# Kernel optimization log

Hardware: AMD Instinct MI355X
Metric: run time of the kernel (lower is better)

The kernel has to match this reference:

```python
import math
import jax, jax.numpy as jnp
import numpy as np

B, S, D, E, K, H = 4, 1024, 768, 8, 2, 2048
NH_ROUTER, NH_COLLAB = 12, 2  # collab heads = min(n_heads, top_k) = 2
EPS = 1e-5


def setup_inputs() -> dict:
    key = jax.random.key(0)
    ks = jax.random.split(key, 16)
    n = lambda k, shp, s=0.02: jax.random.normal(k, shp, jnp.float32) * s
    return {
        "x": jax.random.normal(ks[0], (B, S, D), jnp.float32),
        # parallel expert params (E, D, H) / (E, H, D)
        "w1": n(ks[1], (E, D, H)), "w3": n(ks[2], (E, D, H)), "w2": n(ks[3], (E, H, D)),
        # router self-attention (torch MultiheadAttention packed qkv + out proj)
        "r_in_w": n(ks[4], (3 * D, D)), "r_in_b": jnp.zeros((3 * D,), jnp.float32),
        "r_out_w": n(ks[5], (D, D)), "r_out_b": jnp.zeros((D,), jnp.float32),
        "r_norm_w": jnp.ones((D,), jnp.float32),
        "gate_w": n(ks[6], (E, D)),
        # collaborative cross-attention
        "c_in_w": n(ks[7], (3 * D, D)), "c_in_b": jnp.zeros((3 * D,), jnp.float32),
        "c_out_w": n(ks[8], (D, D)), "c_out_b": jnp.zeros((D,), jnp.float32),
        "c_norm_w": jnp.ones((D,), jnp.float32),
        "ffn_w1": n(ks[9], (D, D)), "ffn_w2": n(ks[10], (D, D)),
        "o_w": n(ks[11], (D, D)),
    }


def _mha(x, in_w, in_b, out_w, out_b, nh):
    # torch nn.MultiheadAttention, batch_first, q=k=v=x; returns out and head-avg probs
    N, L, Dm = x.shape
    hd = Dm // nh
    qkv = x @ in_w.T + in_b                       # (N, L, 3D)
    q, k, v = jnp.split(qkv, 3, axis=-1)
    sp = lambda t: t.reshape(N, L, nh, hd).transpose(0, 2, 1, 3)
    q, k, v = sp(q), sp(k), sp(v)
    probs = jax.nn.softmax(jnp.einsum('nhld,nhmd->nhlm', q, k) / math.sqrt(hd), axis=-1)
    o = jnp.einsum('nhlm,nhmd->nhld', probs, v).transpose(0, 2, 1, 3).reshape(N, L, Dm)
    return o @ out_w.T + out_b, probs.mean(axis=1)


def _rms(x, w):
    return x * jax.lax.rsqrt(jnp.mean(x * x, axis=-1, keepdims=True) + EPS) * w


def reference(x, w1, w3, w2, r_in_w, r_in_b, r_out_w, r_out_b, r_norm_w, gate_w,
              c_in_w, c_in_b, c_out_w, c_out_b, c_norm_w, ffn_w1, ffn_w2, o_w):
    Bx, Sx, Dx = x.shape
    # dense all-expert SwiGLU: (B,S,E,D)
    gate = jnp.einsum('bsd,edh->bseh', x, w1)
    up = jnp.einsum('bsd,edh->bseh', x, w3)
    expert_out = jnp.einsum('bseh,ehd->bsed', jax.nn.silu(gate) * up, w2)
    ef = expert_out.reshape(Bx * Sx, E, Dx)
    # attention-based router over the E experts per token
    ctx, _ = _mha(ef, r_in_w, r_in_b, r_out_w, r_out_b, NH_ROUTER)
    ctx = _rms(ctx + ef, r_norm_w)
    logits = (ctx.mean(axis=1) @ gate_w.T).reshape(Bx, Sx, E)
    routing_probs = jax.nn.softmax(logits, axis=-1)
    tk_logits, tk_idx = jax.lax.top_k(logits, K)  # router_temperature = 1.0
    tk_probs = jax.nn.softmax(tk_logits, axis=-1)
    sel = jnp.take_along_axis(expert_out, tk_idx[..., None], axis=2)  # (B,S,K,D)
    sf = sel.reshape(Bx * Sx, K, Dx)
    # collaborative fusion among selected experts
    ao, aw = _mha(sf, c_in_w, c_in_b, c_out_w, c_out_b, NH_COLLAB)
    ao = _rms(ao + sf, c_norm_w)
    refined = (jax.nn.gelu(ao @ ffn_w1.T, approximate=False) @ ffn_w2.T) + ao
    refined = refined.reshape(Bx, Sx, K, Dx)
    final = jnp.sum(refined * tk_probs[..., None], axis=2) @ o_w.T
    # auxiliary loss
    usage = routing_probs.mean(axis=(0, 1))
    balance = jnp.mean((usage - usage.mean()) ** 2)
    diversity = jnp.mean(-jnp.sum(aw * jnp.log(aw + 1e-9), axis=-1))
    aux = 0.1 * (0.01 * diversity + 0.01 * balance)
    return final, aux, tk_idx
```

## Files before the change

### kernel.cpp

```cpp
#include <hip/hip_runtime.h>


typedef unsigned short u16;
typedef unsigned int u32;
typedef _Float16 f16;
typedef f16 f16x4 __attribute__((ext_vector_type(4)));
typedef f16 f16x8 __attribute__((ext_vector_type(8)));
typedef float f32x4 __attribute__((ext_vector_type(4)));

__device__ __forceinline__ float b2f(u16 v){
  union { u32 u; float f; } x; x.u = ((u32)v) << 16; return x.f;
}
__device__ __forceinline__ u16 f2b(float f){
  union { float f; u32 u; } x; x.f = f;
  u32 u = x.u;
  if ((u & 0x7fffffffu) > 0x7f800000u) return (u16)0x7fc0;
  return (u16)((u + 0x7fffu + ((u >> 16) & 1u)) >> 16);
}
__device__ __forceinline__ float gelu_f(float x){
  return 0.5f * x * (1.f + erff(x * 0.70710678118654752f));
}

template<int NW>
__device__ __forceinline__ float blockReduceSum(float v, float* red){
  #pragma unroll
  for (int o = 32; o > 0; o >>= 1) v += __shfl_down(v, o, 64);
  const int wv = threadIdx.x >> 6, ln = threadIdx.x & 63;
  __syncthreads();
  if (ln == 0) red[wv] = v;
  __syncthreads();
  float s = 0.f;
  #pragma unroll
  for (int i = 0; i < NW; i++) s += red[i];
  return s;
}

template<int AK, bool SPLIT, bool BT, bool BIAS, int ACT, bool RES, bool DUAL, bool SK2>
__global__ __launch_bounds__(256, 2) void mgemm(
    const void* __restrict__ Ap, int lda, long long strideA,
    const float* __restrict__ B1, const float* __restrict__ B2, int ldb, long long strideB,
    float* __restrict__ C1, float* __restrict__ C2, int ldc, long long strideC,
    const float* __restrict__ bias, const float* __restrict__ resid, int ldr,
    int Kd, int zs)
{
  __shared__ f16 AsH[2][128*40];
  __shared__ f16 BsH[2][128*40];
  __shared__ f16 AsL[SPLIT ? 2 : 1][SPLIT ? 128*40 : 4];
  __shared__ f16 BsL[SPLIT ? 2 : 1][SPLIT ? 128*40 : 4];

  const int tid = threadIdx.x;
  const int m0 = blockIdx.y * 128, n0 = blockIdx.x * 128;
  const int z = blockIdx.z;
  int zi = z, k0 = 0, KL = Kd;
  const float* Bz; float* Cz;
  if constexpr (DUAL){
    if (z < zs){ zi = z;      Bz = B1 + (long long)zi*strideB; Cz = C1 + (long long)zi*strideC; }
    else       { zi = z - zs; Bz = B2 + (long long)zi*strideB; Cz = C2 + (long long)zi*strideC; }
  } else if constexpr (SK2){
    const int s = (z >= zs) ? 1 : 0;
    zi = z - s * zs;
    KL = Kd >> 1; k0 = s * KL;
    Bz = B1 + (long long)zi*strideB + (BT ? (long long)k0 : (long long)k0 * ldb);
    Cz = (s ? C2 : C1) + (long long)zi*strideC;
  } else {
    Bz = B1 + (long long)z*strideB; Cz = C1 + (long long)z*strideC;
  }
  const float* A32 = (const float*)Ap + (AK==0 ? (long long)zi*strideA : 0) + k0;
  const u16*   A16 = (const u16*)Ap   + (AK==1 ? (long long)zi*strideA : 0) + k0;

  const int ln = tid & 63, wv = tid >> 6;
  const int wm = (wv >> 1) * 64, wn = (wv & 1) * 64;
  const int fr = ln & 15, fq = ln >> 4;

  const int rA = tid >> 1, kcA = (tid & 1) * 16;
  const int nbB = tid & 31, kbB = tid >> 5;
  const int koB = ((kbB << 2) + ((nbB & 3) << 3)) & 31;

  f32x4 av[4]; uint4 av16[2]; f32x4 bv[4];

  auto loadAB = [&](int kt){
    if constexpr (AK == 0){
      const float* s = A32 + (size_t)(m0 + rA) * lda + kt + kcA;
      av[0] = ((const f32x4*)s)[0]; av[1] = ((const f32x4*)s)[1];
      av[2] = ((const f32x4*)s)[2]; av[3] = ((const f32x4*)s)[3];
    } else {
      const u16* s = A16 + (size_t)(m0 + rA) * lda + kt + kcA;
      av16[0] = ((const uint4*)s)[0]; av16[1] = ((const uint4*)s)[1];
    }
    if constexpr (BT){
      const float* s = Bz + (size_t)(n0 + rA) * ldb + kt + kcA;
      bv[0] = ((const f32x4*)s)[0]; bv[1] = ((const f32x4*)s)[1];
      bv[2] = ((const f32x4*)s)[2]; bv[3] = ((const f32x4*)s)[3];
    } else {
      const float* s = Bz + (size_t)(kt + (kbB << 2)) * ldb + n0 + (nbB << 2);
      bv[0] = *(const f32x4*)(s);
      bv[1] = *(const f32x4*)(s + ldb);
      bv[2] = *(const f32x4*)(s + 2*ldb);
      bv[3] = *(const f32x4*)(s + 3*ldb);
    }
  };

  auto storeAB = [&](int b){
    if constexpr (AK == 0){
      #pragma unroll
      for (int j = 0; j < 4; j++){
        const f32x4 v = av[j];
        f16x4 h;
        #pragma unroll
        for (int c = 0; c < 4; c++) h[c] = (f16)v[c];
        *(f16x4*)&AsH[b][rA*40 + kcA + j*4] = h;
        if constexpr (SPLIT){
          f16x4 l;
          #pragma unroll
          for (int c = 0; c < 4; c++) l[c] = (f16)(v[c] - (float)h[c]);
          *(f16x4*)&AsL[b][rA*40 + kcA + j*4] = l;
        }
      }
    } else {
      #pragma unroll
      for (int j = 0; j < 2; j++){
        const uint4 v = av16[j];
        f16x8 h;
        h[0]=(f16)b2f((u16)(v.x & 0xffff)); h[1]=(f16)b2f((u16)(v.x >> 16));
        h[2]=(f16)b2f((u16)(v.y & 0xffff)); h[3]=(f16)b2f((u16)(v.y >> 16));
        h[4]=(f16)b2f((u16)(v.z & 0xffff)); h[5]=(f16)b2f((u16)(v.z >> 16));
        h[6]=(f16)b2f((u16)(v.w & 0xffff)); h[7]=(f16)b2f((u16)(v.w >> 16));
        *(f16x8*)&AsH[b][rA*40 + kcA + j*8] = h;
      }
    }
    if constexpr (BT){
      #pragma unroll
      for (int j = 0; j < 4; j++){
        const f32x4 v = bv[j];
        f16x4 h;
        #pragma unroll
        for (int c = 0; c < 4; c++) h[c] = (f16)v[c];
        *(f16x4*)&BsH[b][rA*40 + kcA + j*4] = h;
        if constexpr (SPLIT){
          f16x4 l;
          #pragma unroll
          for (int c = 0; c < 4; c++) l[c] = (f16)(v[c] - (float)h[c]);
          *(f16x4*)&BsL[b][rA*40 + kcA + j*4] = l;
        }
      }
    } else {
      #pragma unroll
      for (int c = 0; c < 4; c++){
        const int row = (nbB << 2) + c;
        f16x4 h;
        h[0]=(f16)bv[0][c]; h[1]=(f16)bv[1][c]; h[2]=(f16)bv[2][c]; h[3]=(f16)bv[3][c];
        *(f16x4*)&BsH[b][row*40 + koB] = h;
        if constexpr (SPLIT){
          f16x4 l;
          l[0]=(f16)(bv[0][c]-(float)h[0]); l[1]=(f16)(bv[1][c]-(float)h[1]);
          l[2]=(f16)(bv[2][c]-(float)h[2]); l[3]=(f16)(bv[3][c]-(float)h[3]);
          *(f16x4*)&BsL[b][row*40 + koB] = l;
        }
      }
    }
  };

  f32x4 acc[4][4];
  #pragma unroll
  for (int i = 0; i < 4; i++)
    #pragma unroll
    for (int j = 0; j < 4; j++){ acc[i][j][0]=0.f; acc[i][j][1]=0.f; acc[i][j][2]=0.f; acc[i][j][3]=0.f; }

  int aoff[4], boff[4];
  #pragma unroll
  for (int i = 0; i < 4; i++) aoff[i] = (wm + i*16 + fr)*40 + fq*8;
  #pragma unroll
  for (int j = 0; j < 4; j++){
    const int brow = wn + j*16 + fr;
    boff[j] = brow*40 + (BT ? fq*8 : (((fq + (brow >> 2)) & 3) << 3));
  }

  loadAB(0);
  const int NT = KL >> 5;
  for (int t = 0; t < NT; t++){
    const int b = t & 1;
    storeAB(b);
    __syncthreads();
    if (t + 1 < NT) loadAB((t + 1) << 5);
    f16x8 aH[4], bH[4];
    #pragma unroll
    for (int i = 0; i < 4; i++) aH[i] = *(const f16x8*)&AsH[b][aoff[i]];
    #pragma unroll
    for (int j = 0; j < 4; j++) bH[j] = *(const f16x8*)&BsH[b][boff[j]];
    #pragma unroll
    for (int i = 0; i < 4; i++)
      #pragma unroll
      for (int j = 0; j < 4; j++)
        acc[i][j] = __builtin_amdgcn_mfma_f32_16x16x32_f16(aH[i], bH[j], acc[i][j], 0, 0, 0);
    if constexpr (SPLIT){
      f16x8 aL[4], bL[4];
      #pragma unroll
      for (int i = 0; i < 4; i++) aL[i] = *(const f16x8*)&AsL[b][aoff[i]];
      #pragma unroll
      for (int j = 0; j < 4; j++) bL[j] = *(const f16x8*)&BsL[b][boff[j]];
      #pragma unroll
      for (int i = 0; i < 4; i++)
        #pragma unroll
        for (int j = 0; j < 4; j++){
          acc[i][j] = __builtin_amdgcn_mfma_f32_16x16x32_f16(aH[i], bL[j], acc[i][j], 0, 0, 0);
          acc[i][j] = __builtin_amdgcn_mfma_f32_16x16x32_f16(aL[i], bH[j], acc[i][j], 0, 0, 0);
        }
    }
  }

  #pragma unroll
  for (int j = 0; j < 4; j++){
    const int n = n0 + wn + j*16 + fr;
    float bvv = 0.f;
    if constexpr (BIAS) bvv = bias[n];
    #pragma unroll
    for (int i = 0; i < 4; i++){
      #pragma unroll
      for (int r = 0; r < 4; r++){
        const int m = m0 + wm + i*16 + fq*4 + r;
        float v = acc[i][j][r];
        if constexpr (BIAS) v += bvv;
        if constexpr (ACT == 1) v = gelu_f(v);
        if constexpr (RES) v += resid[(size_t)m * ldr + n];
        Cz[(size_t)m * ldc + n] = v;
      }
    }
  }
}

__global__ void silu_k(const float4* __restrict__ g, const float4* __restrict__ u,
                       float4* __restrict__ h, int n4){
  const int i = blockIdx.x * 256 + threadIdx.x;
  if (i < n4){
    const float4 gv = g[i], uv = u[i];
    float4 r;
    r.x = (gv.x / (1.f + expf(-gv.x))) * uv.x;
    r.y = (gv.y / (1.f + expf(-gv.y))) * uv.y;
    r.z = (gv.z / (1.f + expf(-gv.z))) * uv.z;
    r.w = (gv.w / (1.f + expf(-gv.w))) * uv.w;
    h[i] = r;
  }
}

__global__ void add_k(float* __restrict__ dst, const float* __restrict__ src, int n4){
  const int i = blockIdx.x * 256 + threadIdx.x;
  if (i < n4){
    const f32x4 a = ((const f32x4*)dst)[i];
    const f32x4 b = ((const f32x4*)src)[i];
    f32x4 c; c[0]=a[0]+b[0]; c[1]=a[1]+b[1]; c[2]=a[2]+b[2]; c[3]=a[3]+b[3];
    ((f32x4*)dst)[i] = c;
  }
}

__global__ __launch_bounds__(128) void router_attn(const float* __restrict__ qkv,
                                                   float* __restrict__ attn_o){
  __shared__ float L[8 * 1536];
  __shared__ float Ps[96][8];
  const int t = blockIdx.x, tid = threadIdx.x;
  const float* src = qkv + (size_t)t * 8 * 2304;
  for (int i = tid; i < 3072; i += 128){
    const int e = i / 384, c4 = i - e * 384;
    ((float4*)L)[i] = ((const float4*)(src + (size_t)e * 2304))[c4];
  }
  __syncthreads();
  if (tid < 96){
    const int h = tid >> 3, e = tid & 7;
    const float* q = L + e * 1536 + h * 64;
    float s[8]; float mx = -1e30f;
    #pragma unroll
    for (int e2 = 0; e2 < 8; e2++){
      const float* kk = L + e2 * 1536 + 768 + h * 64;
      float acc = 0.f;
      #pragma unroll
      for (int d = 0; d < 64; d++) acc = fmaf(q[d], kk[d], acc);
      s[e2] = acc * 0.125f;
      mx = fmaxf(mx, s[e2]);
    }
    float den = 0.f;
    #pragma unroll
    for (int e2 = 0; e2 < 8; e2++){ s[e2] = expf(s[e2] - mx); den += s[e2]; }
    const float inv = 1.f / den;
    #pragma unroll
    for (int e2 = 0; e2 < 8; e2++) Ps[tid][e2] = s[e2] * inv;
  }
  __syncthreads();
  for (int i = tid; i < 1536; i += 128){
    const int e = i / 192, c4 = i - e * 192;
    ((float4*)L)[i] = ((const float4*)(src + (size_t)e * 2304 + 1536))[c4];
  }
  __syncthreads();
  if (tid < 96){
    const int h = tid >> 3, e = tid & 7;
    float p[8];
    #pragma unroll
    for (int e2 = 0; e2 < 8; e2++) p[e2] = Ps[tid][e2];
    float* dst = attn_o + ((size_t)t * 8 + e) * 768 + h * 64;
    for (int d = 0; d < 64; d++){
      float acc = 0.f;
      #pragma unroll
      for (int e2 = 0; e2 < 8; e2++) acc = fmaf(p[e2], L[e2 * 768 + h * 64 + d], acc);
      dst[d] = acc;
    }
  }
}

__global__ __launch_bounds__(256) void router_final(
    const float* __restrict__ proj, const float* __restrict__ eoc,
    const float* __restrict__ rnw, const float* __restrict__ gw,
    int t0, float* __restrict__ usage, float* __restrict__ tkp,
    u16* __restrict__ sf, float* __restrict__ oidx)
{
  const int tl = blockIdx.x, t = t0 + tl, tid = threadIdx.x;
  __shared__ float red[4];
  __shared__ float lg[8];
  __shared__ int sidx[2];
  __shared__ float csum[768];
  for (int i = tid; i < 768; i += 256) csum[i] = 0.f;
  __syncthreads();
  for (int e = 0; e < 8; e++){
    const float* pr = proj + ((size_t)tl * 8 + e) * 768;
    const float* er = eoc  + ((size_t)tl * 8 + e) * 768;
    float v[3]; float ss = 0.f;
    #pragma unroll
    for (int i = 0; i < 3; i++){ const int c = tid + i * 256; v[i] = pr[c] + er[c]; ss += v[i] * v[i]; }
    ss = blockReduceSum<4>(ss, red);
    const float sc = 1.f / sqrtf(ss * (1.f / 768.f) + 1e-5f);
    #pragma unroll
    for (int i = 0; i < 3; i++){ const int c = tid + i * 256; csum[c] += v[i] * sc * rnw[c]; }
  }
  for (int j = 0; j < 8; j++){
    float p = 0.f;
    #pragma unroll
    for (int i = 0; i < 3; i++){ const int c = tid + i * 256; p += csum[c] * gw[j * 768 + c]; }
    p = blockReduceSum<4>(p, red);
    if (tid == 0) lg[j] = p * 0.125f;
  }
  __syncthreads();
  if (tid == 0){
    float mx = -1e30f;
    for (int j = 0; j < 8; j++) mx = fmaxf(mx, lg[j]);
    float ex[8], den = 0.f;
    for (int j = 0; j < 8; j++){ ex[j] = expf(lg[j] - mx); den += ex[j]; }
    const float inv = 1.f / den;
    for (int j = 0; j < 8; j++) atomicAdd(&usage[j], ex[j] * inv);
    int i0 = 0; float l0 = lg[0];
    for (int j = 1; j < 8; j++) if (lg[j] > l0){ l0 = lg[j]; i0 = j; }
    int i1 = -1; float l1 = -1e30f;
    for (int j = 0; j < 8; j++) if (j != i0 && lg[j] > l1){ l1 = lg[j]; i1 = j; }
    const float e1 = expf(l1 - l0);
    const float p0 = 1.f / (1.f + e1);
    tkp[(size_t)t * 2]     = p0;
    tkp[(size_t)t * 2 + 1] = e1 * p0;
    sidx[0] = i0; sidx[1] = i1;
    oidx[(size_t)t * 2]     = (float)i0;
    oidx[(size_t)t * 2 + 1] = (float)i1;
  }
  __syncthreads();
  const int i0 = sidx[0], i1 = sidx[1];
  #pragma unroll
  for (int i = 0; i < 3; i++){
    const int c = tid + i * 256;
    sf[((size_t)t * 2 + 0) * 768 + c] = f2b(eoc[((size_t)tl * 8 + i0) * 768 + c]);
    sf[((size_t)t * 2 + 1) * 768 + c] = f2b(eoc[((size_t)tl * 8 + i1) * 768 + c]);
  }
}

__global__ __launch_bounds__(128) void collab_attn(
    const float* __restrict__ qkv, float* __restrict__ attn_o, float* __restrict__ divsum)
{
  const int t = blockIdx.x, tid = threadIdx.x;
  __shared__ float L[4608];
  __shared__ float P[8];
  __shared__ float red[2];
  const float* src = qkv + (size_t)t * 4608;
  for (int i = tid; i < 4608; i += 128) L[i] = src[i];
  __syncthreads();
  for (int hij = 0; hij < 8; hij++){
    const int h = hij >> 2, qi = (hij >> 1) & 1, kj = hij & 1;
    const float* q = L + qi * 2304 + h * 384;
    const float* k = L + kj * 2304 + 768 + h * 384;
    float acc = 0.f;
    for (int d = tid; d < 384; d += 128) acc += q[d] * k[d];
    acc = blockReduceSum<2>(acc, red);
    if (tid == 0) P[hij] = acc;
  }
  __syncthreads();
  if (tid == 0){
    const float scale = 0.051031036307982884f;
    float aw[2][2] = {{0.f,0.f},{0.f,0.f}};
    for (int h = 0; h < 2; h++)
      for (int i = 0; i < 2; i++){
        const float s0 = P[h*4 + i*2 + 0] * scale, s1 = P[h*4 + i*2 + 1] * scale;
        const float m = fmaxf(s0, s1);
        const float e0 = expf(s0 - m), e1 = expf(s1 - m), inv = 1.f / (e0 + e1);
        P[h*4 + i*2 + 0] = e0 * inv; P[h*4 + i*2 + 1] = e1 * inv;
        aw[i][0] += 0.5f * e0 * inv; aw[i][1] += 0.5f * e1 * inv;
      }
    float ent = 0.f;
    for (int i = 0; i < 2; i++)
      for (int j = 0; j < 2; j++) ent -= aw[i][j] * logf(aw[i][j] + 1e-9f);
    atomicAdd(divsum, ent);
  }
  __syncthreads();
  for (int c = tid; c < 768; c += 128){
    const int h = c / 384;
    const float v0 = L[1536 + c], v1 = L[3840 + c];
    attn_o[((size_t)t * 2 + 0) * 768 + c] = P[h*4 + 0] * v0 + P[h*4 + 1] * v1;
    attn_o[((size_t)t * 2 + 1) * 768 + c] = P[h*4 + 2] * v0 + P[h*4 + 3] * v1;
  }
}

__global__ __launch_bounds__(256) void rms_k(const float* __restrict__ a, const u16* __restrict__ b,
                                             const float* __restrict__ wt, float* __restrict__ o){
  const int r = blockIdx.x, tid = threadIdx.x;
  __shared__ float red[4];
  float v[3]; float ss = 0.f;
  #pragma unroll
  for (int i = 0; i < 3; i++){
    const int c = tid + i * 256;
    v[i] = a[(size_t)r * 768 + c] + b2f(b[(size_t)r * 768 + c]);
    ss += v[i] * v[i];
  }
  ss = blockReduceSum<4>(ss, red);
  const float sc = 1.f / sqrtf(ss * (1.f / 768.f) + 1e-5f);
  #pragma unroll
  for (int i = 0; i < 3; i++){
    const int c = tid + i * 256;
    o[(size_t)r * 768 + c] = v[i] * sc * wt[c];
  }
}

__global__ void wsum(const float* __restrict__ refined, const float* __restrict__ tkp,
                     float* __restrict__ y){
  const int idx = blockIdx.x * 256 + threadIdx.x;
  const int t = idx / 768, c = idx - t * 768;
  const float r0 = refined[((size_t)t * 2) * 768 + c];
  const float r1 = refined[((size_t)t * 2 + 1) * 768 + c];
  y[idx] = tkp[t * 2] * r0 + tkp[t * 2 + 1] * r1;
}

__global__ void aux_k(const float* __restrict__ usage, const float* __restrict__ divsum,
                      float* __restrict__ out){
  if (threadIdx.x == 0 && blockIdx.x == 0){
    float u[8], s = 0.f;
    for (int e = 0; e < 8; e++){ u[e] = usage[e] * (1.f / 4096.f); s += u[e]; }
    const float mean = s * 0.125f;
    float bal = 0.f;
    for (int e = 0; e < 8; e++){ const float d = u[e] - mean; bal += d * d; }
    bal *= 0.125f;
    const float div = divsum[0] * (1.f / 8192.f);
    out[0] = 0.1f * (0.01f * div + 0.01f * bal);
  }
}

__global__ void zero_k(float* p, int n){
  const int i = blockIdx.x * 64 + threadIdx.x;
  if (i < n) p[i] = 0.f;
}

extern "C" void kernel_launch(void* const* d_in, const int* in_sizes, int n_in,
                              void* d_out, int out_size, void* d_ws, size_t ws_size,
                              hipStream_t stream)
{
  (void)in_sizes; (void)n_in; (void)out_size; (void)ws_size;
  const float* x       = (const float*)d_in[0];
  const float* w1      = (const float*)d_in[1];
  const float* w3      = (const float*)d_in[2];
  const float* w2      = (const float*)d_in[3];
  const float* r_in_w  = (const float*)d_in[4];
  const float* r_in_b  = (const float*)d_in[5];
  const float* r_out_w = (const float*)d_in[6];
  const float* r_out_b = (const float*)d_in[7];
  const float* r_norm_w= (const float*)d_in[8];
  const float* gate_w  = (const float*)d_in[9];
  const float* c_in_w  = (const float*)d_in[10];
  const float* c_in_b  = (const float*)d_in[11];
  const float* c_out_w = (const float*)d_in[12];
  const float* c_out_b = (const float*)d_in[13];
  const float* c_norm_w= (const float*)d_in[14];
  const float* ffn_w1  = (const float*)d_in[15];
  const float* ffn_w2  = (const float*)d_in[16];
  const float* o_w     = (const float*)d_in[17];

  char* wsb   = (char*)d_ws;
  char* arena = wsb;
  float* eoc  = (float*)(wsb + 33554432);
  u16*   sf   = (u16*)  (wsb + 39845888);
  float* tkp  = (float*)(wsb + 52428800);
  float* usage= (float*)(wsb + 52461568);

  float* gateb = (float*)(arena);
  float* upb   = (float*)(arena + 16777216);
  float* qkvr  = (float*)(arena);
  float* aor   = (float*)(arena + 18874368);
  float* projr = (float*)(arena + 25165824);

  float* qkvc  = (float*)(arena);
  float* aoc   = (float*)(arena + 18874368);
  float* projc = (float*)(arena + 25165824);
  float* aob   = (float*)(arena);
  float* t1b   = (float*)(arena + 6291456);
  float* refb  = (float*)(arena + 12582912);
  float* ybuf  = (float*)(arena + 18874368);

  float* outp    = (float*)d_out;
  float* out_aux = outp + (size_t)4096*768;
  float* out_idx = out_aux + 1;

  zero_k<<<1, 64, 0, stream>>>(usage, 16);

  for (int cch = 0; cch < 16; cch++){
    const int t0 = cch * 256;
    mgemm<0,true,false,false,0,false,true,false><<<dim3(16,2,16),256,0,stream>>>(
      x + (size_t)t0*768, 768, 0LL,
      w1, w3, 2048, 1572864LL,
      gateb, upb, 2048, 524288LL,
      nullptr, nullptr, 0, 768, 8);
    silu_k<<<4096, 256, 0, stream>>>((const float4*)gateb, (const float4*)upb,
                                     (float4*)gateb, 1048576);
    mgemm<0,true,false,false,0,false,false,true><<<dim3(6,2,16),256,0,stream>>>(
      gateb, 2048, 524288LL,
      w2, nullptr, 768, 1572864LL,
      eoc, upb, 6144, 768LL,
      nullptr, nullptr, 0, 2048, 8);
    add_k<<<1536, 256, 0, stream>>>(eoc, upb, 393216);
    mgemm<0,true,true,true,0,false,false,false><<<dim3(18,16,1),256,0,stream>>>(
      eoc, 768, 0LL, r_in_w, nullptr, 768, 0LL,
      qkvr, nullptr, 2304, 0LL, r_in_b, nullptr, 0, 768, 0);
    router_attn<<<256, 128, 0, stream>>>(qkvr, aor);
    mgemm<0,true,true,true,0,false,false,false><<<dim3(6,16,1),256,0,stream>>>(
      aor, 768, 0LL, r_out_w, nullptr, 768, 0LL,
      projr, nullptr, 768, 0LL, r_out_b, nullptr, 0, 768, 0);
    router_final<<<256, 256, 0, stream>>>(projr, eoc, r_norm_w, gate_w, t0,
                                          usage, tkp, sf, out_idx);
  }

  for (int q = 0; q < 4; q++){
    const int tq0 = q * 1024;
    const u16* sf_q = sf + (size_t)tq0 * 2 * 768;
    mgemm<1,false,true,true,0,false,false,false><<<dim3(18,16,1),256,0,stream>>>(
      sf_q, 768, 0LL, c_in_w, nullptr, 768, 0LL,
      qkvc, nullptr, 2304, 0LL, c_in_b, nullptr, 0, 768, 0);
    collab_attn<<<1024, 128, 0, stream>>>(qkvc, aoc, usage + 8);
    mgemm<0,false,true,true,0,false,false,false><<<dim3(6,16,1),256,0,stream>>>(
      aoc, 768, 0LL, c_out_w, nullptr, 768, 0LL,
      projc, nullptr, 768, 0LL, c_out_b, nullptr, 0, 768, 0);
    rms_k<<<2048, 256, 0, stream>>>(projc, sf_q, c_norm_w, aob);
    mgemm<0,false,true,false,1,false,false,false><<<dim3(6,16,1),256,0,stream>>>(
      aob, 768, 0LL, ffn_w1, nullptr, 768, 0LL,
      t1b, nullptr, 768, 0LL, nullptr, nullptr, 0, 768, 0);
    mgemm<0,false,true,false,0,true,false,false><<<dim3(6,16,1),256,0,stream>>>(
      t1b, 768, 0LL, ffn_w2, nullptr, 768, 0LL,
      refb, nullptr, 768, 0LL, nullptr, aob, 768, 768, 0);
    wsum<<<3072, 256, 0, stream>>>(refb, tkp + (size_t)tq0 * 2, ybuf);
    mgemm<0,false,true,false,0,false,false,true><<<dim3(6,8,2),256,0,stream>>>(
      ybuf, 768, 0LL, o_w, nullptr, 768, 0LL,
      outp + (size_t)tq0 * 768, t1b, 768, 0LL, nullptr, nullptr, 0, 768, 1);
    add_k<<<768, 256, 0, stream>>>(outp + (size_t)tq0 * 768, t1b, 196608);
  }
  aux_k<<<1, 64, 0, stream>>>(usage, usage + 8, out_aux);
}
```

Baseline: 4.486 ms.

## Split-K small GEMMs, widen smem stores, wave-per-token router_final

Several unrelated changes land together. The 768x768 projection and FFN GEMMs now use split-K over two z-slices, with a new fused add/bias/GELU/residual elementwise kernel that combines the partial sums, so the grid doubles from 96 blocks to 192. The mgemm shared-memory staging is rewritten to write 8-wide f16 vectors, and the non-transposed B loads now read 8 rows of float2 per thread. router_final moves from one block per token to one wavefront per token using shuffle reductions. Together these aim to raise occupancy and cut LDS and sync overhead. The cost is extra elementwise passes and scratch traffic through reused buffers.

```diff
diff --git a/kernel.cpp b/kernel.cpp
--- a/kernel.cpp
+++ b/kernel.cpp
@@ -33,6 +33,12 @@
   #pragma unroll
   for (int i = 0; i < NW; i++) s += red[i];
   return s;
+}
+
+__device__ __forceinline__ float waveReduceSum(float v){
+  #pragma unroll
+  for (int o = 32; o > 0; o >>= 1) v += __shfl_xor(v, o, 64);
+  return v;
 }
 
 template<int AK, bool SPLIT, bool BT, bool BIAS, int ACT, bool RES, bool DUAL, bool SK2>
@@ -73,10 +79,9 @@
   const int fr = ln & 15, fq = ln >> 4;
 
   const int rA = tid >> 1, kcA = (tid & 1) * 16;
-  const int nbB = tid & 31, kbB = tid >> 5;
-  const int koB = ((kbB << 2) + ((nbB & 3) << 3)) & 31;
-
-  f32x4 av[4]; uint4 av16[2]; f32x4 bv[4];
+  const int npB = tid & 63, kgB = tid >> 6;
+
+  f32x4 av[4]; uint4 av16[2]; f32x4 bv[4]; float2 bw[8];
 
   auto loadAB = [&](int kt){
     if constexpr (AK == 0){
@@ -92,29 +97,25 @@
       bv[0] = ((const f32x4*)s)[0]; bv[1] = ((const f32x4*)s)[1];
       bv[2] = ((const f32x4*)s)[2]; bv[3] = ((const f32x4*)s)[3];
     } else {
-      const float* s = Bz + (size_t)(kt + (kbB << 2)) * ldb + n0 + (nbB << 2);
-      bv[0] = *(const f32x4*)(s);
-      bv[1] = *(const f32x4*)(s + ldb);
-      bv[2] = *(const f32x4*)(s + 2*ldb);
-      bv[3] = *(const f32x4*)(s + 3*ldb);
+      const float* s = Bz + (size_t)(kt + kgB * 8) * ldb + n0 + 2 * npB;
+      #pragma unroll
+      for (int kk = 0; kk < 8; kk++) bw[kk] = *(const float2*)(s + (size_t)kk * ldb);
     }
   };
 
   auto storeAB = [&](int b){
     if constexpr (AK == 0){
       #pragma unroll
-      for (int j = 0; j < 4; j++){
-        const f32x4 v = av[j];
-        f16x4 h;
+      for (int jj = 0; jj < 2; jj++){
+        f16x8 h, l;
         #pragma unroll
-        for (int c = 0; c < 4; c++) h[c] = (f16)v[c];
-        *(f16x4*)&AsH[b][rA*40 + kcA + j*4] = h;
-        if constexpr (SPLIT){
-          f16x4 l;
-          #pragma unroll
-          for (int c = 0; c < 4; c++) l[c] = (f16)(v[c] - (float)h[c]);
-          *(f16x4*)&AsL[b][rA*40 + kcA + j*4] = l;
+        for (int c = 0; c < 8; c++){
+          const float v = av[jj*2 + (c>>2)][c & 3];
+          h[c] = (f16)v;
+          if constexpr (SPLIT) l[c] = (f16)(v - (float)h[c]);
         }
+        *(f16x8*)&AsH[b][rA*40 + kcA + jj*8] = h;
+        if constexpr (SPLIT) *(f16x8*)&AsL[b][rA*40 + kcA + jj*8] = l;
       }
     } else {
       #pragma unroll
@@ -130,32 +131,31 @@
     }
     if constexpr (BT){
       #pragma unroll
-      for (int j = 0; j < 4; j++){
-        const f32x4 v = bv[j];
-        f16x4 h;
+      for (int jj = 0; jj < 2; jj++){
+        f16x8 h, l;
         #pragma unroll
-        for (int c = 0; c < 4; c++) h[c] = (f16)v[c];
-        *(f16x4*)&BsH[b][rA*40 + kcA + j*4] = h;
-        if constexpr (SPLIT){
-          f16x4 l;
-          #pragma unroll
-          for (int c = 0; c < 4; c++) l[c] = (f16)(v[c] - (float)h[c]);
-          *(f16x4*)&BsL[b][rA*40 + kcA + j*4] = l;
+        for (int c = 0; c < 8; c++){
+          const float v = bv[jj*2 + (c>>2)][c & 3];
+          h[c] = (f16)v;
+          if constexpr (SPLIT) l[c] = (f16)(v - (float)h[c]);
         }
+        *(f16x8*)&BsH[b][rA*40 + kcA + jj*8] = h;
+        if constexpr (SPLIT) *(f16x8*)&BsL[b][rA*40 + kcA + jj*8] = l;
       }
     } else {
       #pragma unroll
-      for (int c = 0; c < 4; c++){
-        const int row = (nbB << 2) + c;
-        f16x4 h;
-        h[0]=(f16)bv[0][c]; h[1]=(f16)bv[1][c]; h[2]=(f16)bv[2][c]; h[3]=(f16)bv[3][c];
-        *(f16x4*)&BsH[b][row*40 + koB] = h;
-        if constexpr (SPLIT){
-          f16x4 l;
-          l[0]=(f16)(bv[0][c]-(float)h[0]); l[1]=(f16)(bv[1][c]-(float)h[1]);
-          l[2]=(f16)(bv[2][c]-(float)h[2]); l[3]=(f16)(bv[3][c]-(float)h[3]);
-          *(f16x4*)&BsL[b][row*40 + koB] = l;
+      for (int c = 0; c < 2; c++){
+        const int row = 2*npB + c;
+        const int p8 = (kgB + (row >> 2)) & 3;
+        f16x8 h, l;
+        #pragma unroll
+        for (int kk = 0; kk < 8; kk++){
+          const float v = c ? bw[kk].y : bw[kk].x;
+          h[kk] = (f16)v;
+          if constexpr (SPLIT) l[kk] = (f16)(v - (float)h[kk]);
         }
+        *(f16x8*)&BsH[b][row*40 + p8*8] = h;
+        if constexpr (SPLIT) *(f16x8*)&BsL[b][row*40 + p8*8] = l;
       }
     }
   };
@@ -242,14 +242,25 @@
   }
 }
 
-__global__ void add_k(float* __restrict__ dst, const float* __restrict__ src, int n4){
+template<int ACT, bool RES, bool BIAS>
+__global__ void add2_k(float* __restrict__ dst, const float* __restrict__ src,
+                       const float* __restrict__ bias, const float* __restrict__ resid,
+                       int n4, int ld4){
   const int i = blockIdx.x * 256 + threadIdx.x;
-  if (i < n4){
-    const f32x4 a = ((const f32x4*)dst)[i];
-    const f32x4 b = ((const f32x4*)src)[i];
-    f32x4 c; c[0]=a[0]+b[0]; c[1]=a[1]+b[1]; c[2]=a[2]+b[2]; c[3]=a[3]+b[3];
-    ((f32x4*)dst)[i] = c;
-  }
+  if (i >= n4) return;
+  const f32x4 a = ((const f32x4*)dst)[i];
+  const f32x4 b = ((const f32x4*)src)[i];
+  const int c4 = (i % ld4) * 4;
+  f32x4 r;
+  #pragma unroll
+  for (int c = 0; c < 4; c++){
+    float v = a[c] + b[c];
+    if constexpr (BIAS) v += bias[c4 + c];
+    if constexpr (ACT == 1) v = gelu_f(v);
+    if constexpr (RES) v += resid[(size_t)i * 4 + c];
+    r[c] = v;
+  }
+  ((f32x4*)dst)[i] = r;
 }
 
 __global__ __launch_bounds__(128) void router_attn(const float* __restrict__ qkv,
@@ -310,58 +321,88 @@
     int t0, float* __restrict__ usage, float* __restrict__ tkp,
     u16* __restrict__ sf, float* __restrict__ oidx)
 {
-  const int tl = blockIdx.x, t = t0 + tl, tid = threadIdx.x;
-  __shared__ float red[4];
-  __shared__ float lg[8];
-  __shared__ int sidx[2];
-  __shared__ float csum[768];
-  for (int i = tid; i < 768; i += 256) csum[i] = 0.f;
-  __syncthreads();
+  const int wv = threadIdx.x >> 6, ln = threadIdx.x & 63;
+  const int tl = blockIdx.x * 4 + wv, t = t0 + tl;
+
+  float rw[12];
+  #pragma unroll
+  for (int g = 0; g < 3; g++){
+    const f32x4 w = ((const f32x4*)rnw)[ln + g * 64];
+    #pragma unroll
+    for (int c = 0; c < 4; c++) rw[g*4 + c] = w[c];
+  }
+
+  float cs[12];
+  #pragma unroll
+  for (int i = 0; i < 12; i++) cs[i] = 0.f;
+
   for (int e = 0; e < 8; e++){
     const float* pr = proj + ((size_t)tl * 8 + e) * 768;
     const float* er = eoc  + ((size_t)tl * 8 + e) * 768;
-    float v[3]; float ss = 0.f;
-    #pragma unroll
-    for (int i = 0; i < 3; i++){ const int c = tid + i * 256; v[i] = pr[c] + er[c]; ss += v[i] * v[i]; }
-    ss = blockReduceSum<4>(ss, red);
+    float v[12]; float ss = 0.f;
+    #pragma unroll
+    for (int g = 0; g < 3; g++){
+      const f32x4 a = ((const f32x4*)pr)[ln + g * 64];
+      const f32x4 b = ((const f32x4*)er)[ln + g * 64];
+      #pragma unroll
+      for (int c = 0; c < 4; c++){ const float vv = a[c] + b[c]; v[g*4 + c] = vv; ss += vv * vv; }
+    }
+    ss = waveReduceSum(ss);
     const float sc = 1.f / sqrtf(ss * (1.f / 768.f) + 1e-5f);
     #pragma unroll
-    for (int i = 0; i < 3; i++){ const int c = tid + i * 256; csum[c] += v[i] * sc * rnw[c]; }
-  }
+    for (int i = 0; i < 12; i++) cs[i] += v[i] * sc * rw[i];
+  }
+
+  float lg[8];
+  #pragma unroll
   for (int j = 0; j < 8; j++){
+    const float* gwr = gw + j * 768;
     float p = 0.f;
     #pragma unroll
-    for (int i = 0; i < 3; i++){ const int c = tid + i * 256; p += csum[c] * gw[j * 768 + c]; }
-    p = blockReduceSum<4>(p, red);
-    if (tid == 0) lg[j] = p * 0.125f;
-  }
-  __syncthreads();
-  if (tid == 0){
+    for (int g = 0; g < 3; g++){
+      const f32x4 w = ((const f32x4*)gwr)[ln + g * 64];
+      #pragma unroll
+      for (int c = 0; c < 4; c++) p += cs[g*4 + c] * w[c];
+    }
+    lg[j] = waveReduceSum(p) * 0.125f;
+  }
+
+  int i0 = 0; float l0 = lg[0];
+  #pragma unroll
+  for (int j = 1; j < 8; j++) if (lg[j] > l0){ l0 = lg[j]; i0 = j; }
+  int i1 = -1; float l1 = -1e30f;
+  #pragma unroll
+  for (int j = 0; j < 8; j++) if (j != i0 && lg[j] > l1){ l1 = lg[j]; i1 = j; }
+
+  if (ln == 0){
     float mx = -1e30f;
+    #pragma unroll
     for (int j = 0; j < 8; j++) mx = fmaxf(mx, lg[j]);
     float ex[8], den = 0.f;
+    #pragma unroll
     for (int j = 0; j < 8; j++){ ex[j] = expf(lg[j] - mx); den += ex[j]; }
     const float inv = 1.f / den;
+    #pragma unroll
     for (int j = 0; j < 8; j++) atomicAdd(&usage[j], ex[j] * inv);
-    int i0 = 0; float l0 = lg[0];
-    for (int j = 1; j < 8; j++) if (lg[j] > l0){ l0 = lg[j]; i0 = j; }
-    int i1 = -1; float l1 = -1e30f;
-    for (int j = 0; j < 8; j++) if (j != i0 && lg[j] > l1){ l1 = lg[j]; i1 = j; }
     const float e1 = expf(l1 - l0);
     const float p0 = 1.f / (1.f + e1);
     tkp[(size_t)t * 2]     = p0;
     tkp[(size_t)t * 2 + 1] = e1 * p0;
-    sidx[0] = i0; sidx[1] = i1;
     oidx[(size_t)t * 2]     = (float)i0;
     oidx[(size_t)t * 2 + 1] = (float)i1;
   }
-  __syncthreads();
-  const int i0 = sidx[0], i1 = sidx[1];
-  #pragma unroll
-  for (int i = 0; i < 3; i++){
-    const int c = tid + i * 256;
-    sf[((size_t)t * 2 + 0) * 768 + c] = f2b(eoc[((size_t)tl * 8 + i0) * 768 + c]);
-    sf[((size_t)t * 2 + 1) * 768 + c] = f2b(eoc[((size_t)tl * 8 + i1) * 768 + c]);
+
+  #pragma unroll
+  for (int s = 0; s < 2; s++){
+    const int ie = s ? i1 : i0;
+    const float* er = eoc + ((size_t)tl * 8 + ie) * 768;
+    #pragma unroll
+    for (int g = 0; g < 3; g++){
+      const f32x4 a = ((const f32x4*)er)[ln + g * 64];
+      ushort4 o;
+      o.x = f2b(a[0]); o.y = f2b(a[1]); o.z = f2b(a[2]); o.w = f2b(a[3]);
+      *(ushort4*)&sf[((size_t)t * 2 + s) * 768 + 4 * (ln + g * 64)] = o;
+    }
   }
 }
 
@@ -523,16 +564,17 @@
       w2, nullptr, 768, 1572864LL,
       eoc, upb, 6144, 768LL,
       nullptr, nullptr, 0, 2048, 8);
-    add_k<<<1536, 256, 0, stream>>>(eoc, upb, 393216);
+    add2_k<0,false,false><<<1536, 256, 0, stream>>>(eoc, upb, nullptr, nullptr, 393216, 192);
     mgemm<0,true,true,true,0,false,false,false><<<dim3(18,16,1),256,0,stream>>>(
       eoc, 768, 0LL, r_in_w, nullptr, 768, 0LL,
       qkvr, nullptr, 2304, 0LL, r_in_b, nullptr, 0, 768, 0);
     router_attn<<<256, 128, 0, stream>>>(qkvr, aor);
-    mgemm<0,true,true,true,0,false,false,false><<<dim3(6,16,1),256,0,stream>>>(
+    mgemm<0,true,true,false,0,false,false,true><<<dim3(6,16,2),256,0,stream>>>(
       aor, 768, 0LL, r_out_w, nullptr, 768, 0LL,
-      projr, nullptr, 768, 0LL, r_out_b, nullptr, 0, 768, 0);
-    router_final<<<256, 256, 0, stream>>>(projr, eoc, r_norm_w, gate_w, t0,
-                                          usage, tkp, sf, out_idx);
+      projr, qkvr, 768, 0LL, nullptr, nullptr, 0, 768, 1);
+    add2_k<0,false,true><<<1536, 256, 0, stream>>>(projr, qkvr, r_out_b, nullptr, 393216, 192);
+    router_final<<<64, 256, 0, stream>>>(projr, eoc, r_norm_w, gate_w, t0,
+                                         usage, tkp, sf, out_idx);
   }
 
   for (int q = 0; q < 4; q++){
@@ -542,21 +584,24 @@
       sf_q, 768, 0LL, c_in_w, nullptr, 768, 0LL,
       qkvc, nullptr, 2304, 0LL, c_in_b, nullptr, 0, 768, 0);
     collab_attn<<<1024, 128, 0, stream>>>(qkvc, aoc, usage + 8);
-    mgemm<0,false,true,true,0,false,false,false><<<dim3(6,16,1),256,0,stream>>>(
+    mgemm<0,false,true,false,0,false,false,true><<<dim3(6,16,2),256,0,stream>>>(
       aoc, 768, 0LL, c_out_w, nullptr, 768, 0LL,
-      projc, nullptr, 768, 0LL, c_out_b, nullptr, 0, 768, 0);
+      projc, qkvc, 768, 0LL, nullptr, nullptr, 0, 768, 1);
+    add2_k<0,false,true><<<1536, 256, 0, stream>>>(projc, qkvc, c_out_b, nullptr, 393216, 192);
     rms_k<<<2048, 256, 0, stream>>>(projc, sf_q, c_norm_w, aob);
-    mgemm<0,false,true,false,1,false,false,false><<<dim3(6,16,1),256,0,stream>>>(
+    mgemm<0,false,true,false,0,false,false,true><<<dim3(6,16,2),256,0,stream>>>(
       aob, 768, 0LL, ffn_w1, nullptr, 768, 0LL,
-      t1b, nullptr, 768, 0LL, nullptr, nullptr, 0, 768, 0);
-    mgemm<0,false,true,false,0,true,false,false><<<dim3(6,16,1),256,0,stream>>>(
+      t1b, refb, 768, 0LL, nullptr, nullptr, 0, 768, 1);
+    add2_k<1,false,false><<<1536, 256, 0, stream>>>(t1b, refb, nullptr, nullptr, 393216, 192);
+    mgemm<0,false,true,false,0,false,false,true><<<dim3(6,16,2),256,0,stream>>>(
       t1b, 768, 0LL, ffn_w2, nullptr, 768, 0LL,
-      refb, nullptr, 768, 0LL, nullptr, aob, 768, 768, 0);
+      refb, projc, 768, 0LL, nullptr, nullptr, 0, 768, 1);
+    add2_k<0,true,false><<<1536, 256, 0, stream>>>(refb, projc, nullptr, aob, 393216, 192);
     wsum<<<3072, 256, 0, stream>>>(refb, tkp + (size_t)tq0 * 2, ybuf);
     mgemm<0,false,true,false,0,false,false,true><<<dim3(6,8,2),256,0,stream>>>(
       ybuf, 768, 0LL, o_w, nullptr, 768, 0LL,
       outp + (size_t)tq0 * 768, t1b, 768, 0LL, nullptr, nullptr, 0, 768, 1);
-    add_k<<<768, 256, 0, stream>>>(outp + (size_t)tq0 * 768, t1b, 196608);
+    add2_k<0,false,false><<<768, 256, 0, stream>>>(outp + (size_t)tq0 * 768, t1b, nullptr, nullptr, 196608, 192);
   }
   aux_k<<<1, 64, 0, stream>>>(usage, usage + 8, out_aux);
 }
```

Result: faster. 4.209 ms (-6.2%).
